# Kernel optimization log

Hardware: AMD Instinct MI355X
Metric: run time of the kernel (lower is better)

The kernel has to match this reference:

```python
import jax, jax.numpy as jnp
import numpy as np
import math

B, S, D, H, F = 2, 2048, 1024, 16, 4096
HD = D // H  # head size 64
EPS = 1e-5


def layernorm(x, g, b):
    mu = jnp.mean(x, axis=-1, keepdims=True)
    var = jnp.mean((x - mu) ** 2, axis=-1, keepdims=True)
    return (x - mu) * jax.lax.rsqrt(var + EPS) * g + b


def new_gelu(x):
    c = math.sqrt(2.0 / math.pi)
    return 0.5 * x * (1.0 + jnp.tanh(c * (x + 0.044715 * x ** 3)))


def setup_inputs() -> dict:
    key = jax.random.key(0)
    ks = jax.random.split(key, 20)
    sc = 0.02
    return {
        "x": jax.random.normal(ks[0], (B, S, D), jnp.float32),
        # per-head q/k/v weights stacked: [H, HD, D] (torch Linear weight layout [out,in])
        "Wq": jax.random.normal(ks[1], (H, HD, D), jnp.float32) * sc,
        "bq": jax.random.normal(ks[2], (H, HD), jnp.float32) * sc,
        "Wk": jax.random.normal(ks[3], (H, HD, D), jnp.float32) * sc,
        "bk": jax.random.normal(ks[4], (H, HD), jnp.float32) * sc,
        "Wv": jax.random.normal(ks[5], (H, HD, D), jnp.float32) * sc,
        "bv": jax.random.normal(ks[6], (H, HD), jnp.float32) * sc,
        "Wo": jax.random.normal(ks[7], (D, D), jnp.float32) * sc,
        "bo": jax.random.normal(ks[8], (D,), jnp.float32) * sc,
        "ln1_g": 1.0 + jax.random.normal(ks[9], (D,), jnp.float32) * sc,
        "ln1_b": jax.random.normal(ks[10], (D,), jnp.float32) * sc,
        "W1": jax.random.normal(ks[11], (F, D), jnp.float32) * sc,
        "b1": jax.random.normal(ks[12], (F,), jnp.float32) * sc,
        "W2": jax.random.normal(ks[13], (D, F), jnp.float32) * sc,
        "b2": jax.random.normal(ks[14], (D,), jnp.float32) * sc,
        "ln2_g": 1.0 + jax.random.normal(ks[15], (D,), jnp.float32) * sc,
        "ln2_b": jax.random.normal(ks[16], (D,), jnp.float32) * sc,
    }


def reference(x, Wq, bq, Wk, bk, Wv, bv, Wo, bo, ln1_g, ln1_b, W1, b1, W2, b2, ln2_g, ln2_b):
    # --- pre-LN multi-head attention (dropout is identity in eval) ---
    h = layernorm(x, ln1_g, ln1_b)
    q = jnp.einsum("bsd,hed->bshe", h, Wq) + bq  # [B,S,H,HD]
    k = jnp.einsum("bsd,hed->bshe", h, Wk) + bk
    v = jnp.einsum("bsd,hed->bshe", h, Wv) + bv
    scores = jnp.einsum("bshe,bthe->bhst", q, k) / math.sqrt(HD)
    probs = jax.nn.softmax(scores, axis=-1)
    attn = jnp.einsum("bhst,bthe->bshe", probs, v).reshape(B, S, D)  # concat heads
    attn = attn @ Wo.T + bo
    x = x + attn
    # --- pre-LN MLP with NewGELU ---
    h2 = layernorm(x, ln2_g, ln2_b)
    mlp = new_gelu(h2 @ W1.T + b1) @ W2.T + b2
    return x + mlp
```

## Files before the change

### kernel.cpp

```cpp
#include <hip/hip_runtime.h>

typedef unsigned short u16;
typedef __attribute__((ext_vector_type(8))) __bf16 bf16x8;
typedef __attribute__((ext_vector_type(4))) __bf16 bf16x4;
typedef __attribute__((ext_vector_type(4))) float f32x4;
typedef __attribute__((ext_vector_type(4))) unsigned short u16x4;

#define AS1 __attribute__((address_space(1)))
#define AS3 __attribute__((address_space(3)))

__device__ __forceinline__ void async_load16(const void* g, void* l) {
  __builtin_amdgcn_global_load_lds((const AS1 void*)g, (AS3 void*)l, 16, 0, 0);
}

__device__ __forceinline__ float exp2_fast(float x) {
#if __has_builtin(__builtin_amdgcn_exp2f)
  return __builtin_amdgcn_exp2f(x);
#else
  return exp2f(x);
#endif
}
__device__ __forceinline__ float rcp_fast(float x) {
#if __has_builtin(__builtin_amdgcn_rcpf)
  return __builtin_amdgcn_rcpf(x);
#else
  return 1.0f / x;
#endif
}

__device__ __forceinline__ u16 f2bf(float f) {
  union { float f; unsigned u; } a; a.f = f;
  unsigned u = a.u;
  u += 0x7fffu + ((u >> 16) & 1u);
  return (u16)(u >> 16);
}
__device__ __forceinline__ u16 bf_bits(float f) {
  union { __bf16 b; u16 u; } c; c.b = (__bf16)f; return c.u;
}
__device__ __forceinline__ float bf2f(u16 h) {
  union { unsigned u; float f; } c; c.u = ((unsigned)h) << 16; return c.f;
}

__global__ __launch_bounds__(256)
void f2b_all(const float* __restrict__ s0, const float* __restrict__ s1,
             const float* __restrict__ s2, const float* __restrict__ s3,
             const float* __restrict__ s4, const float* __restrict__ s5,
             u16* __restrict__ dst) {
  const int i = blockIdx.x * 256 + threadIdx.x;
  const float* s; int off;
  if (i < 1048576) {
    if (i < 262144)      { s = s0; off = i; }
    else if (i < 524288) { s = s1; off = i - 262144; }
    else if (i < 786432) { s = s2; off = i - 524288; }
    else                 { s = s3; off = i - 786432; }
  } else if (i < 2097152) { s = s4; off = i - 1048576; }
  else                    { s = s5; off = i - 2097152; }
  const float4 v = ((const float4*)s)[off];
  u16x4 o; o[0] = f2bf(v.x); o[1] = f2bf(v.y); o[2] = f2bf(v.z); o[3] = f2bf(v.w);
  ((u16x4*)dst)[i] = o;
}

__global__ __launch_bounds__(256)
void ln_kernel(const float* __restrict__ x, const float* __restrict__ g,
               const float* __restrict__ b, u16* __restrict__ out) {
  const int row = blockIdx.x, tid = threadIdx.x;
  const float4 v = ((const float4*)(x + (size_t)row * 1024))[tid];
  float s = v.x + v.y + v.z + v.w;
  float s2 = v.x * v.x + v.y * v.y + v.z * v.z + v.w * v.w;
#pragma unroll
  for (int o = 1; o < 64; o <<= 1) { s += __shfl_xor(s, o); s2 += __shfl_xor(s2, o); }
  __shared__ float red[8];
  const int wave = tid >> 6, lane = tid & 63;
  if (lane == 0) { red[wave] = s; red[wave + 4] = s2; }
  __syncthreads();
  s = red[0] + red[1] + red[2] + red[3];
  s2 = red[4] + red[5] + red[6] + red[7];
  const float mu = s * (1.f / 1024.f);
  const float rstd = rsqrtf(s2 * (1.f / 1024.f) - mu * mu + 1e-5f);
  const float4 gg = ((const float4*)g)[tid];
  const float4 bb = ((const float4*)b)[tid];
  u16x4 o4;
  o4[0] = f2bf((v.x - mu) * rstd * gg.x + bb.x);
  o4[1] = f2bf((v.y - mu) * rstd * gg.y + bb.y);
  o4[2] = f2bf((v.z - mu) * rstd * gg.z + bb.z);
  o4[3] = f2bf((v.w - mu) * rstd * gg.w + bb.w);
  ((u16x4*)(out + (size_t)row * 1024))[tid] = o4;
}

__global__ __launch_bounds__(256)
void ln_fuse(const float* __restrict__ x, const u16* __restrict__ parts,
             const float* __restrict__ bo, const float* __restrict__ g,
             const float* __restrict__ b, float* __restrict__ out,
             u16* __restrict__ hb) {
  const int row = blockIdx.x, tid = threadIdx.x;
  const size_t base = (size_t)row * 1024;
  const int i4 = row * 256 + tid;
  const float4 xv = ((const float4*)(x + base))[tid];
  const u16x4 h0 = ((const u16x4*)parts)[i4];
  const u16x4 h1 = ((const u16x4*)(parts + 4194304))[i4];
  const float4 bv = ((const float4*)bo)[tid];
  float4 t;
  t.x = xv.x + bf2f(h0[0]) + bf2f(h1[0]) + bv.x;
  t.y = xv.y + bf2f(h0[1]) + bf2f(h1[1]) + bv.y;
  t.z = xv.z + bf2f(h0[2]) + bf2f(h1[2]) + bv.z;
  t.w = xv.w + bf2f(h0[3]) + bf2f(h1[3]) + bv.w;
  ((float4*)(out + base))[tid] = t;
  float s = t.x + t.y + t.z + t.w;
  float s2 = t.x * t.x + t.y * t.y + t.z * t.z + t.w * t.w;
#pragma unroll
  for (int o = 1; o < 64; o <<= 1) { s += __shfl_xor(s, o); s2 += __shfl_xor(s2, o); }
  __shared__ float red[8];
  const int wave = tid >> 6, lane = tid & 63;
  if (lane == 0) { red[wave] = s; red[wave + 4] = s2; }
  __syncthreads();
  s = red[0] + red[1] + red[2] + red[3];
  s2 = red[4] + red[5] + red[6] + red[7];
  const float mu = s * (1.f / 1024.f);
  const float rstd = rsqrtf(s2 * (1.f / 1024.f) - mu * mu + 1e-5f);
  const float4 gg = ((const float4*)g)[tid];
  const float4 bb = ((const float4*)b)[tid];
  u16x4 o4;
  o4[0] = f2bf((t.x - mu) * rstd * gg.x + bb.x);
  o4[1] = f2bf((t.y - mu) * rstd * gg.y + bb.y);
  o4[2] = f2bf((t.z - mu) * rstd * gg.z + bb.z);
  o4[3] = f2bf((t.w - mu) * rstd * gg.w + bb.w);
  ((u16x4*)(hb + base))[tid] = o4;
}

__global__ __launch_bounds__(256)
void add4(float* __restrict__ out, const u16* __restrict__ p,
          const float* __restrict__ b2) {
  const int i = blockIdx.x * 256 + threadIdx.x;
  const float4 o = ((const float4*)out)[i];
  const float4 bv = ((const float4*)b2)[i & 255];
  float a0 = o.x + bv.x, a1 = o.y + bv.y, a2 = o.z + bv.z, a3 = o.w + bv.w;
#pragma unroll
  for (int kz = 0; kz < 4; kz++) {
    const u16x4 h = ((const u16x4*)(p + (size_t)kz * 4194304))[i];
    a0 += bf2f(h[0]); a1 += bf2f(h[1]); a2 += bf2f(h[2]); a3 += bf2f(h[3]);
  }
  float4 r; r.x = a0; r.y = a1; r.z = a2; r.w = a3;
  ((float4*)out)[i] = r;
}

template <class Epi>
__global__ __launch_bounds__(256, 2)
void gemm_bt(const u16* __restrict__ A, const u16* __restrict__ Bw,
             int ldk, int K, int NB, Epi epi) {
  __shared__ __align__(16) u16 As[256 * 32];
  __shared__ __align__(16) u16 Bs[128 * 32];
  const int tid = threadIdx.x;
  const int wave = tid >> 6, lane = tid & 63;
  const int quad = lane >> 4, l16 = lane & 15;
  const int id = blockIdx.x;
  const int mb = id & 15;
  const int t = id >> 4;
  const int nb = t % NB;
  const int kz = t / NB;
  const int bm = mb * 256, bn = nb * 128;
  const int wm = wave * 64;

  const int srow = lane >> 2, scol = (lane & 3) * 8;
  const u16* pa[4];
  u16* la[4];
#pragma unroll
  for (int j = 0; j < 4; j++) {
    pa[j] = A + (size_t)(bm + wave * 64 + j * 16 + srow) * ldk + (size_t)kz * K + scol;
    la[j] = &As[wave * 2048 + j * 512];
  }
  const u16* pb[2];
  u16* lb[2];
#pragma unroll
  for (int j = 0; j < 2; j++) {
    pb[j] = Bw + (size_t)(bn + wave * 32 + j * 16 + srow) * ldk + (size_t)kz * K + scol;
    lb[j] = &Bs[wave * 1024 + j * 512];
  }

  const f32x4 fz = {0.f, 0.f, 0.f, 0.f};
  f32x4 acc[4][8];
#pragma unroll
  for (int i = 0; i < 4; i++)
#pragma unroll
    for (int j = 0; j < 8; j++) acc[i][j] = fz;

  for (int k0 = 0; k0 < K; k0 += 32) {
#pragma unroll
    for (int j = 0; j < 4; j++) { async_load16(pa[j], la[j]); pa[j] += 32; }
#pragma unroll
    for (int j = 0; j < 2; j++) { async_load16(pb[j], lb[j]); pb[j] += 32; }
    __syncthreads();
    bf16x8 af[4], bfr[8];
#pragma unroll
    for (int mi = 0; mi < 4; mi++)
      af[mi] = *(const bf16x8*)&As[(wm + mi * 16 + l16) * 32 + quad * 8];
#pragma unroll
    for (int ni = 0; ni < 8; ni++)
      bfr[ni] = *(const bf16x8*)&Bs[(ni * 16 + l16) * 32 + quad * 8];
#pragma unroll
    for (int mi = 0; mi < 4; mi++)
#pragma unroll
      for (int ni = 0; ni < 8; ni++)
        acc[mi][ni] = __builtin_amdgcn_mfma_f32_16x16x32_bf16(af[mi], bfr[ni], acc[mi][ni], 0, 0, 0);
    __syncthreads();
  }
#pragma unroll
  for (int mi = 0; mi < 4; mi++)
#pragma unroll
    for (int ni = 0; ni < 8; ni++)
      epi(bm + wm + mi * 16 + quad * 4, bn + ni * 16 + l16, kz, acc[mi][ni]);
}

struct EpiQKV {
  u16 *q, *k, *vt; const float *bq, *bk, *bv;
  __device__ void operator()(int m0, int n, int, f32x4 v) const {
    const int which = n >> 10, nn = n & 1023;
    const int hh = nn >> 6, e = nn & 63;
    const int bb = m0 >> 11, s0 = m0 & 2047;
    const size_t bh = (size_t)(bb * 16 + hh);
    if (which == 0) {
      const float bias = bq[nn];
      u16* p = &q[(bh * 2048 + s0) * 64 + e];
#pragma unroll
      for (int r = 0; r < 4; r++) p[r * 64] = bf_bits((v[r] + bias) * 0.18033688f);
    } else if (which == 1) {
      const float bias = bk[nn];
      u16* p = &k[(bh * 2048 + s0) * 64 + e];
#pragma unroll
      for (int r = 0; r < 4; r++) p[r * 64] = bf_bits(v[r] + bias);
    } else {
      const float bias = bv[nn];
      bf16x4 pk;
#pragma unroll
      for (int r = 0; r < 4; r++) pk[r] = (__bf16)(v[r] + bias);
      *(bf16x4*)&vt[(bh * 64 + e) * 2048 + s0] = pk;
    }
  }
};
struct EpiPartB {
  u16* p;
  __device__ void operator()(int m0, int n, int kz, f32x4 v) const {
    u16* pp = p + (size_t)kz * 4194304;
#pragma unroll
    for (int r = 0; r < 4; r++) pp[(size_t)(m0 + r) * 1024 + n] = bf_bits(v[r]);
  }
};
struct EpiGelu {
  const float* b1; u16* o;
  __device__ void operator()(int m0, int n, int, f32x4 v) const {
    const float bias = b1[n];
#pragma unroll
    for (int r = 0; r < 4; r++) {
      const float u = v[r] + bias;
      const float z2 = u * (2.3021183f + 0.10294515f * u * u);
      const float d = 1.0f + exp2_fast(-z2);
      o[(size_t)(m0 + r) * 4096 + n] = bf_bits(u * rcp_fast(d));
    }
  }
};

__global__ __launch_bounds__(256)
void attn_kernel(const u16* __restrict__ Q, const u16* __restrict__ K,
                 const u16* __restrict__ Vt, u16* __restrict__ O) {
  __shared__ __align__(16) u16 Ks[64 * 72];
  __shared__ __align__(16) u16 Vs[64 * 72];
  __shared__ __align__(16) u16 Ps[4][32 * 72];
  const int tid = threadIdx.x, wave = tid >> 6, lane = tid & 63;
  const int quad = lane >> 4, l16 = lane & 15;
  const int b = blockIdx.z, h = blockIdx.y, qt = blockIdx.x;
  const size_t bh = (size_t)(b * 16 + h);
  const u16* Qp = Q + bh * (size_t)(2048 * 64);
  const u16* Kp = K + bh * (size_t)(2048 * 64);
  const u16* Vp = Vt + bh * (size_t)(64 * 2048);
  const int q0 = qt * 128 + wave * 32;

  bf16x8 qf[2][2];
#pragma unroll
  for (int rg = 0; rg < 2; rg++) {
    const u16* qrow = &Qp[(size_t)(q0 + rg * 16 + l16) * 64 + quad * 8];
    qf[rg][0] = *(const bf16x8*)qrow;
    qf[rg][1] = *(const bf16x8*)(qrow + 32);
  }

  const int sr = tid >> 2, sc = (tid & 3) * 16;
  const int krow = 4 * (sr & 15) + (sr >> 4);
  const u16* kg = &Kp[(size_t)krow * 64 + sc];
  const u16* vg = &Vp[(size_t)sr * 2048 + sc];
  u16* kl = &Ks[sr * 72 + sc];
  u16* vl = &Vs[sr * 72 + sc];
  u16* Pw = &Ps[wave][0];

  bf16x8 ones;
#pragma unroll
  for (int i = 0; i < 8; i++) ones[i] = (__bf16)1.0f;

  const f32x4 fz = {0.f, 0.f, 0.f, 0.f};
  f32x4 acc[2][4], lsum[2];
#pragma unroll
  for (int rg = 0; rg < 2; rg++) {
    lsum[rg] = fz;
#pragma unroll
    for (int g = 0; g < 4; g++) acc[rg][g] = fz;
  }

  bf16x8 pk0 = *(const bf16x8*)kg, pk1 = *(const bf16x8*)(kg + 8);
  bf16x8 pv0 = *(const bf16x8*)vg, pv1 = *(const bf16x8*)(vg + 8);

  for (int t0 = 0; t0 < 2048; t0 += 64) {
    *(bf16x8*)kl = pk0; *(bf16x8*)(kl + 8) = pk1;
    *(bf16x8*)vl = pv0; *(bf16x8*)(vl + 8) = pv1;
    __syncthreads();
    kg += 64 * 64; vg += 64;
    pk0 = *(const bf16x8*)kg; pk1 = *(const bf16x8*)(kg + 8);
    pv0 = *(const bf16x8*)vg; pv1 = *(const bf16x8*)(vg + 8);

    f32x4 s[2][4];
#pragma unroll
    for (int g = 0; g < 4; g++) {
      const u16* kr = &Ks[(g * 16 + l16) * 72 + quad * 8];
      const bf16x8 kb0 = *(const bf16x8*)kr;
      const bf16x8 kb1 = *(const bf16x8*)(kr + 32);
#pragma unroll
      for (int rg = 0; rg < 2; rg++) {
        f32x4 z = __builtin_amdgcn_mfma_f32_16x16x32_bf16(qf[rg][0], kb0, fz, 0, 0, 0);
        s[rg][g] = __builtin_amdgcn_mfma_f32_16x16x32_bf16(qf[rg][1], kb1, z, 0, 0, 0);
      }
    }
#pragma unroll
    for (int rg = 0; rg < 2; rg++)
#pragma unroll
      for (int r = 0; r < 4; r++) {
        f32x4 pf;
#pragma unroll
        for (int g = 0; g < 4; g++) pf[g] = exp2_fast(s[rg][g][r]);
        const bf16x4 pb = __builtin_convertvector(pf, bf16x4);
        *(bf16x4*)&Pw[(rg * 16 + quad * 4 + r) * 72 + 4 * l16] = pb;
      }
    bf16x8 pa[2][2];
#pragma unroll
    for (int rg = 0; rg < 2; rg++) {
      const u16* pr = &Pw[(rg * 16 + l16) * 72 + quad * 8];
      pa[rg][0] = *(const bf16x8*)pr;
      pa[rg][1] = *(const bf16x8*)(pr + 32);
      lsum[rg] = __builtin_amdgcn_mfma_f32_16x16x32_bf16(pa[rg][0], ones, lsum[rg], 0, 0, 0);
      lsum[rg] = __builtin_amdgcn_mfma_f32_16x16x32_bf16(pa[rg][1], ones, lsum[rg], 0, 0, 0);
    }
#pragma unroll
    for (int g = 0; g < 4; g++) {
      const u16* vr = &Vs[(g * 16 + l16) * 72 + quad * 8];
      const bf16x8 vb0 = *(const bf16x8*)vr;
      const bf16x8 vb1 = *(const bf16x8*)(vr + 32);
#pragma unroll
      for (int rg = 0; rg < 2; rg++) {
        acc[rg][g] = __builtin_amdgcn_mfma_f32_16x16x32_bf16(pa[rg][0], vb0, acc[rg][g], 0, 0, 0);
        acc[rg][g] = __builtin_amdgcn_mfma_f32_16x16x32_bf16(pa[rg][1], vb1, acc[rg][g], 0, 0, 0);
      }
    }
    __syncthreads();
  }
#pragma unroll
  for (int rg = 0; rg < 2; rg++)
#pragma unroll
    for (int r = 0; r < 4; r++) {
      const float inv = rcp_fast(lsum[rg][r]);
      const int s_row = q0 + rg * 16 + quad * 4 + r;
      u16* op = (u16*)&O[((size_t)(b * 2048 + s_row)) * 1024 + h * 64 + l16];
#pragma unroll
      for (int g = 0; g < 4; g++) op[g * 16] = bf_bits(acc[rg][g][r] * inv);
    }
}

extern "C" void kernel_launch(void* const* d_in, const int* in_sizes, int n_in,
                              void* d_out, int out_size, void* d_ws, size_t ws_size,
                              hipStream_t stream) {
  const float* x   = (const float*)d_in[0];
  const float* Wq  = (const float*)d_in[1];
  const float* bq  = (const float*)d_in[2];
  const float* Wk  = (const float*)d_in[3];
  const float* bk  = (const float*)d_in[4];
  const float* Wv  = (const float*)d_in[5];
  const float* bv  = (const float*)d_in[6];
  const float* Wo  = (const float*)d_in[7];
  const float* bo  = (const float*)d_in[8];
  const float* g1  = (const float*)d_in[9];
  const float* be1 = (const float*)d_in[10];
  const float* W1  = (const float*)d_in[11];
  const float* b1  = (const float*)d_in[12];
  const float* W2  = (const float*)d_in[13];
  const float* b2  = (const float*)d_in[14];
  const float* g2  = (const float*)d_in[15];
  const float* be2 = (const float*)d_in[16];
  float* out = (float*)d_out;

  char* w = (char*)d_ws;
  u16* wqkv = (u16*)w; w += (size_t)3072 * 1024 * 2;
  u16* wob  = (u16*)w; w += (size_t)1024 * 1024 * 2;
  u16* w1b  = (u16*)w; w += (size_t)4096 * 1024 * 2;
  u16* w2b  = (u16*)w; w += (size_t)1024 * 4096 * 2;
  u16* hb   = (u16*)w; w += (size_t)4096 * 1024 * 2;
  u16* qb   = (u16*)w; w += (size_t)4096 * 1024 * 2;
  u16* kb   = (u16*)w; w += (size_t)4096 * 1024 * 2;
  u16* vtb  = (u16*)w; w += (size_t)4096 * 1024 * 2;
  u16* atb  = (u16*)w; w += (size_t)4096 * 1024 * 2;
  u16* m1b  = (u16*)w; w += (size_t)4096 * 4096 * 2;

  u16* op_part = m1b;
  u16* ml_part = qb;

  f2b_all<<<12288, 256, 0, stream>>>(Wq, Wk, Wv, Wo, W1, W2, wqkv);

  ln_kernel<<<4096, 256, 0, stream>>>(x, g1, be1, hb);
  gemm_bt<EpiQKV><<<384, 256, 0, stream>>>(hb, wqkv, 1024, 1024, 24,
      EpiQKV{qb, kb, vtb, bq, bk, bv});
  attn_kernel<<<dim3(16, 16, 2), 256, 0, stream>>>(qb, kb, vtb, atb);
  gemm_bt<EpiPartB><<<256, 256, 0, stream>>>(atb, wob, 1024, 512, 8,
      EpiPartB{op_part});
  ln_fuse<<<4096, 256, 0, stream>>>(x, op_part, bo, g2, be2, out, hb);
  gemm_bt<EpiGelu><<<512, 256, 0, stream>>>(hb, w1b, 1024, 1024, 32,
      EpiGelu{b1, m1b});
  gemm_bt<EpiPartB><<<512, 256, 0, stream>>>(m1b, w2b, 4096, 1024, 8,
      EpiPartB{ml_part});
  add4<<<4096, 256, 0, stream>>>(out, ml_part, b2);
}
```

Measured before the change: 360.3 us.

## Halve attention query tile per wave to double grid size

Each wave in the attention kernel now handles 16 query rows instead of 32, so a block covers 64 queries and the grid doubles to 32x16x2 blocks. The goal is more blocks to fill the GPU's compute units, with fewer registers and less shared memory per block so more waves can be resident. In exchange, every K/V tile is loaded from global memory into LDS twice as often overall, and each K/V fragment read from LDS feeds half as many MFMAs.

```diff
diff --git a/kernel.cpp b/kernel.cpp
--- a/kernel.cpp
+++ b/kernel.cpp
@@ -263,7 +263,7 @@
                  const u16* __restrict__ Vt, u16* __restrict__ O) {
   __shared__ __align__(16) u16 Ks[64 * 72];
   __shared__ __align__(16) u16 Vs[64 * 72];
-  __shared__ __align__(16) u16 Ps[4][32 * 72];
+  __shared__ __align__(16) u16 Ps[4][16 * 72];
   const int tid = threadIdx.x, wave = tid >> 6, lane = tid & 63;
   const int quad = lane >> 4, l16 = lane & 15;
   const int b = blockIdx.z, h = blockIdx.y, qt = blockIdx.x;
@@ -271,14 +271,13 @@
   const u16* Qp = Q + bh * (size_t)(2048 * 64);
   const u16* Kp = K + bh * (size_t)(2048 * 64);
   const u16* Vp = Vt + bh * (size_t)(64 * 2048);
-  const int q0 = qt * 128 + wave * 32;
-
-  bf16x8 qf[2][2];
-#pragma unroll
-  for (int rg = 0; rg < 2; rg++) {
-    const u16* qrow = &Qp[(size_t)(q0 + rg * 16 + l16) * 64 + quad * 8];
-    qf[rg][0] = *(const bf16x8*)qrow;
-    qf[rg][1] = *(const bf16x8*)(qrow + 32);
+  const int q0 = qt * 64 + wave * 16;
+
+  bf16x8 qf0, qf1;
+  {
+    const u16* qrow = &Qp[(size_t)(q0 + l16) * 64 + quad * 8];
+    qf0 = *(const bf16x8*)qrow;
+    qf1 = *(const bf16x8*)(qrow + 32);
   }
 
   const int sr = tid >> 2, sc = (tid & 3) * 16;
@@ -294,13 +293,9 @@
   for (int i = 0; i < 8; i++) ones[i] = (__bf16)1.0f;
 
   const f32x4 fz = {0.f, 0.f, 0.f, 0.f};
-  f32x4 acc[2][4], lsum[2];
-#pragma unroll
-  for (int rg = 0; rg < 2; rg++) {
-    lsum[rg] = fz;
-#pragma unroll
-    for (int g = 0; g < 4; g++) acc[rg][g] = fz;
-  }
+  f32x4 acc[4], lsum = fz;
+#pragma unroll
+  for (int g = 0; g < 4; g++) acc[g] = fz;
 
   bf16x8 pk0 = *(const bf16x8*)kg, pk1 = *(const bf16x8*)(kg + 8);
   bf16x8 pv0 = *(const bf16x8*)vg, pv1 = *(const bf16x8*)(vg + 8);
@@ -313,60 +308,49 @@
     pk0 = *(const bf16x8*)kg; pk1 = *(const bf16x8*)(kg + 8);
     pv0 = *(const bf16x8*)vg; pv1 = *(const bf16x8*)(vg + 8);
 
-    f32x4 s[2][4];
+    f32x4 s[4];
 #pragma unroll
     for (int g = 0; g < 4; g++) {
       const u16* kr = &Ks[(g * 16 + l16) * 72 + quad * 8];
       const bf16x8 kb0 = *(const bf16x8*)kr;
       const bf16x8 kb1 = *(const bf16x8*)(kr + 32);
-#pragma unroll
-      for (int rg = 0; rg < 2; rg++) {
-        f32x4 z = __builtin_amdgcn_mfma_f32_16x16x32_bf16(qf[rg][0], kb0, fz, 0, 0, 0);
-        s[rg][g] = __builtin_amdgcn_mfma_f32_16x16x32_bf16(qf[rg][1], kb1, z, 0, 0, 0);
-      }
-    }
-#pragma unroll
-    for (int rg = 0; rg < 2; rg++)
-#pragma unroll
-      for (int r = 0; r < 4; r++) {
-        f32x4 pf;
-#pragma unroll
-        for (int g = 0; g < 4; g++) pf[g] = exp2_fast(s[rg][g][r]);
-        const bf16x4 pb = __builtin_convertvector(pf, bf16x4);
-        *(bf16x4*)&Pw[(rg * 16 + quad * 4 + r) * 72 + 4 * l16] = pb;
-      }
-    bf16x8 pa[2][2];
-#pragma unroll
-    for (int rg = 0; rg < 2; rg++) {
-      const u16* pr = &Pw[(rg * 16 + l16) * 72 + quad * 8];
-      pa[rg][0] = *(const bf16x8*)pr;
-      pa[rg][1] = *(const bf16x8*)(pr + 32);
-      lsum[rg] = __builtin_amdgcn_mfma_f32_16x16x32_bf16(pa[rg][0], ones, lsum[rg], 0, 0, 0);
-      lsum[rg] = __builtin_amdgcn_mfma_f32_16x16x32_bf16(pa[rg][1], ones, lsum[rg], 0, 0, 0);
-    }
+      f32x4 z = __builtin_amdgcn_mfma_f32_16x16x32_bf16(qf0, kb0, fz, 0, 0, 0);
+      s[g] = __builtin_amdgcn_mfma_f32_16x16x32_bf16(qf1, kb1, z, 0, 0, 0);
+    }
+#pragma unroll
+    for (int r = 0; r < 4; r++) {
+      f32x4 pf;
+#pragma unroll
+      for (int g = 0; g < 4; g++) pf[g] = exp2_fast(s[g][r]);
+      const bf16x4 pb = __builtin_convertvector(pf, bf16x4);
+      *(bf16x4*)&Pw[(quad * 4 + r) * 72 + 4 * l16] = pb;
+    }
+    bf16x8 pa0, pa1;
+    {
+      const u16* pr = &Pw[l16 * 72 + quad * 8];
+      pa0 = *(const bf16x8*)pr;
+      pa1 = *(const bf16x8*)(pr + 32);
+    }
+    lsum = __builtin_amdgcn_mfma_f32_16x16x32_bf16(pa0, ones, lsum, 0, 0, 0);
+    lsum = __builtin_amdgcn_mfma_f32_16x16x32_bf16(pa1, ones, lsum, 0, 0, 0);
 #pragma unroll
     for (int g = 0; g < 4; g++) {
       const u16* vr = &Vs[(g * 16 + l16) * 72 + quad * 8];
       const bf16x8 vb0 = *(const bf16x8*)vr;
       const bf16x8 vb1 = *(const bf16x8*)(vr + 32);
-#pragma unroll
-      for (int rg = 0; rg < 2; rg++) {
-        acc[rg][g] = __builtin_amdgcn_mfma_f32_16x16x32_bf16(pa[rg][0], vb0, acc[rg][g], 0, 0, 0);
-        acc[rg][g] = __builtin_amdgcn_mfma_f32_16x16x32_bf16(pa[rg][1], vb1, acc[rg][g], 0, 0, 0);
-      }
+      acc[g] = __builtin_amdgcn_mfma_f32_16x16x32_bf16(pa0, vb0, acc[g], 0, 0, 0);
+      acc[g] = __builtin_amdgcn_mfma_f32_16x16x32_bf16(pa1, vb1, acc[g], 0, 0, 0);
     }
     __syncthreads();
   }
 #pragma unroll
-  for (int rg = 0; rg < 2; rg++)
-#pragma unroll
-    for (int r = 0; r < 4; r++) {
-      const float inv = rcp_fast(lsum[rg][r]);
-      const int s_row = q0 + rg * 16 + quad * 4 + r;
-      u16* op = (u16*)&O[((size_t)(b * 2048 + s_row)) * 1024 + h * 64 + l16];
-#pragma unroll
-      for (int g = 0; g < 4; g++) op[g * 16] = bf_bits(acc[rg][g][r] * inv);
-    }
+  for (int r = 0; r < 4; r++) {
+    const float inv = rcp_fast(lsum[r]);
+    const int s_row = q0 + quad * 4 + r;
+    u16* op = (u16*)&O[((size_t)(b * 2048 + s_row)) * 1024 + h * 64 + l16];
+#pragma unroll
+    for (int g = 0; g < 4; g++) op[g * 16] = bf_bits(acc[g][r] * inv);
+  }
 }
 
 extern "C" void kernel_launch(void* const* d_in, const int* in_sizes, int n_in,
@@ -411,7 +395,7 @@
   ln_kernel<<<4096, 256, 0, stream>>>(x, g1, be1, hb);
   gemm_bt<EpiQKV><<<384, 256, 0, stream>>>(hb, wqkv, 1024, 1024, 24,
       EpiQKV{qb, kb, vtb, bq, bk, bv});
-  attn_kernel<<<dim3(16, 16, 2), 256, 0, stream>>>(qb, kb, vtb, atb);
+  attn_kernel<<<dim3(32, 16, 2), 256, 0, stream>>>(qb, kb, vtb, atb);
   gemm_bt<EpiPartB><<<256, 256, 0, stream>>>(atb, wob, 1024, 512, 8,
       EpiPartB{op_part});
   ln_fuse<<<4096, 256, 0, stream>>>(x, op_part, bo, g2, be2, out, hb);
```

After: 368.2 us. +2.2%, slower.

## Replace GEMM with 8-wave 256x256 double-buffered pipelined kernel and swizzled LDS

Applied to the files above, without the earlier changes.

Replaces the 4-wave 256x128 GEMM, which synchronises on every 32-wide k-step, with an 8-wave 256x256 tile. The new kernel stages 64-wide k tiles through a double-buffered LDS ring with async loads, XOR-swizzles LDS addresses, and uses explicit barriers, waitcnts and setprio to overlap loads with MFMA. The output-projection split-K goes from 2 to 4 parts, and ln_fuse now sums four partials. Attention MFMA sections also gain setprio hints. The larger tiles cut LDS and global traffic per MFMA, at the cost of fewer blocks and more partial-sum traffic for the output projection.

```diff
diff --git a/kernel.cpp b/kernel.cpp
--- a/kernel.cpp
+++ b/kernel.cpp
@@ -96,14 +96,14 @@
   const size_t base = (size_t)row * 1024;
   const int i4 = row * 256 + tid;
   const float4 xv = ((const float4*)(x + base))[tid];
-  const u16x4 h0 = ((const u16x4*)parts)[i4];
-  const u16x4 h1 = ((const u16x4*)(parts + 4194304))[i4];
   const float4 bv = ((const float4*)bo)[tid];
   float4 t;
-  t.x = xv.x + bf2f(h0[0]) + bf2f(h1[0]) + bv.x;
-  t.y = xv.y + bf2f(h0[1]) + bf2f(h1[1]) + bv.y;
-  t.z = xv.z + bf2f(h0[2]) + bf2f(h1[2]) + bv.z;
-  t.w = xv.w + bf2f(h0[3]) + bf2f(h1[3]) + bv.w;
+  t.x = xv.x + bv.x; t.y = xv.y + bv.y; t.z = xv.z + bv.z; t.w = xv.w + bv.w;
+#pragma unroll
+  for (int kz = 0; kz < 4; kz++) {
+    const u16x4 h = ((const u16x4*)(parts + (size_t)kz * 4194304))[i4];
+    t.x += bf2f(h[0]); t.y += bf2f(h[1]); t.z += bf2f(h[2]); t.w += bf2f(h[3]);
+  }
   ((float4*)(out + base))[tid] = t;
   float s = t.x + t.y + t.z + t.w;
   float s2 = t.x * t.x + t.y * t.y + t.z * t.z + t.w * t.w;
@@ -144,70 +144,132 @@
 }
 
 template <class Epi>
-__global__ __launch_bounds__(256, 2)
-void gemm_bt(const u16* __restrict__ A, const u16* __restrict__ Bw,
-             int ldk, int K, int NB, Epi epi) {
-  __shared__ __align__(16) u16 As[256 * 32];
-  __shared__ __align__(16) u16 Bs[128 * 32];
+__global__ __launch_bounds__(512, 2)
+void gemm8(const u16* __restrict__ A, const u16* __restrict__ Bw,
+           int ldk, int K, int NB, Epi epi) {
+  __shared__ __align__(16) u16 lds[65536];
   const int tid = threadIdx.x;
-  const int wave = tid >> 6, lane = tid & 63;
+  const int lane = tid & 63, wave = tid >> 6;
   const int quad = lane >> 4, l16 = lane & 15;
+  const int wmh = wave >> 2, wn = wave & 3;
   const int id = blockIdx.x;
   const int mb = id & 15;
   const int t = id >> 4;
   const int nb = t % NB;
   const int kz = t / NB;
-  const int bm = mb * 256, bn = nb * 128;
-  const int wm = wave * 64;
-
-  const int srow = lane >> 2, scol = (lane & 3) * 8;
-  const u16* pa[4];
-  u16* la[4];
-#pragma unroll
-  for (int j = 0; j < 4; j++) {
-    pa[j] = A + (size_t)(bm + wave * 64 + j * 16 + srow) * ldk + (size_t)kz * K + scol;
-    la[j] = &As[wave * 2048 + j * 512];
-  }
-  const u16* pb[2];
-  u16* lb[2];
-#pragma unroll
-  for (int j = 0; j < 2; j++) {
-    pb[j] = Bw + (size_t)(bn + wave * 32 + j * 16 + srow) * ldk + (size_t)kz * K + scol;
-    lb[j] = &Bs[wave * 1024 + j * 512];
-  }
-
+  const int bm = mb * 256, bn = nb * 256;
+  const int ntile = K >> 6;
+  const int iters = ntile >> 1;
+
+  const int srow = tid >> 3;
+  const int scol = ((tid & 7) * 8) ^ (((tid >> 5) & 1) << 4);
+  const size_t ldkz = (size_t)ldk;
+  const u16* Ag = A + (size_t)(bm + srow) * ldkz + (size_t)kz * K + scol;
+  const u16* Bg = Bw + (size_t)(bn + srow) * ldkz + (size_t)kz * K + scol;
+
+#define STAGE(kt, hf) do { \
+    const u16* gp_ = (((hf) & 2) ? Bg : Ag) + (size_t)(((hf) & 1) * 128) * ldkz + (size_t)(kt) * 64; \
+    u16* lp_ = &lds[(((hf) & 2) ? 32768 : 0) + (((kt) & 1) * 2 + ((hf) & 1)) * 8192 + wave * 512]; \
+    async_load16(gp_, lp_); \
+    async_load16(gp_ + 64 * ldkz, lp_ + 4096); \
+  } while (0)
+#define STG(kt, hf) do { if ((kt) >= 2 && (kt) < ntile) STAGE(kt, hf); } while (0)
+
+  const int qsw = (quad ^ (2 * ((l16 >> 2) & 1))) * 8;
+  const int fro = l16 * 64 + qsw;
+  const u16* aB0 = &lds[(0 * 2 + wmh) * 8192];
+  const u16* aB1 = &lds[(1 * 2 + wmh) * 8192];
+  const u16* bB0 = &lds[32768 + (0 * 2 + (wn >> 1)) * 8192 + (wn & 1) * 4096];
+  const u16* bB1 = &lds[32768 + (1 * 2 + (wn >> 1)) * 8192 + (wn & 1) * 4096];
+
+  bf16x8 aF[4][2], bF[4][2];
   const f32x4 fz = {0.f, 0.f, 0.f, 0.f};
-  f32x4 acc[4][8];
-#pragma unroll
-  for (int i = 0; i < 4; i++)
-#pragma unroll
-    for (int j = 0; j < 8; j++) acc[i][j] = fz;
-
-  for (int k0 = 0; k0 < K; k0 += 32) {
-#pragma unroll
-    for (int j = 0; j < 4; j++) { async_load16(pa[j], la[j]); pa[j] += 32; }
-#pragma unroll
-    for (int j = 0; j < 2; j++) { async_load16(pb[j], lb[j]); pb[j] += 32; }
-    __syncthreads();
-    bf16x8 af[4], bfr[8];
-#pragma unroll
-    for (int mi = 0; mi < 4; mi++)
-      af[mi] = *(const bf16x8*)&As[(wm + mi * 16 + l16) * 32 + quad * 8];
-#pragma unroll
-    for (int ni = 0; ni < 8; ni++)
-      bfr[ni] = *(const bf16x8*)&Bs[(ni * 16 + l16) * 32 + quad * 8];
-#pragma unroll
-    for (int mi = 0; mi < 4; mi++)
-#pragma unroll
-      for (int ni = 0; ni < 8; ni++)
-        acc[mi][ni] = __builtin_amdgcn_mfma_f32_16x16x32_bf16(af[mi], bfr[ni], acc[mi][ni], 0, 0, 0);
-    __syncthreads();
-  }
-#pragma unroll
-  for (int mi = 0; mi < 4; mi++)
-#pragma unroll
-    for (int ni = 0; ni < 8; ni++)
-      epi(bm + wm + mi * 16 + quad * 4, bn + ni * 16 + l16, kz, acc[mi][ni]);
+  f32x4 acc[8][4];
+#pragma unroll
+  for (int m = 0; m < 8; m++)
+#pragma unroll
+    for (int n = 0; n < 4; n++) acc[m][n] = fz;
+
+#define LDAH(ab, mq) do { \
+    aF[0][0] = *(const bf16x8*)&(ab)[fro + ((mq)*4 + 0) * 1024];      \
+    aF[0][1] = *(const bf16x8*)&(ab)[fro + ((mq)*4 + 0) * 1024 + 32]; \
+    aF[1][0] = *(const bf16x8*)&(ab)[fro + ((mq)*4 + 1) * 1024];      \
+    aF[1][1] = *(const bf16x8*)&(ab)[fro + ((mq)*4 + 1) * 1024 + 32]; \
+    aF[2][0] = *(const bf16x8*)&(ab)[fro + ((mq)*4 + 2) * 1024];      \
+    aF[2][1] = *(const bf16x8*)&(ab)[fro + ((mq)*4 + 2) * 1024 + 32]; \
+    aF[3][0] = *(const bf16x8*)&(ab)[fro + ((mq)*4 + 3) * 1024];      \
+    aF[3][1] = *(const bf16x8*)&(ab)[fro + ((mq)*4 + 3) * 1024 + 32]; \
+  } while (0)
+#define LDBH(bb, nq) do { \
+    bF[(nq)*2 + 0][0] = *(const bf16x8*)&(bb)[fro + ((nq)*2 + 0) * 1024];      \
+    bF[(nq)*2 + 0][1] = *(const bf16x8*)&(bb)[fro + ((nq)*2 + 0) * 1024 + 32]; \
+    bF[(nq)*2 + 1][0] = *(const bf16x8*)&(bb)[fro + ((nq)*2 + 1) * 1024];      \
+    bF[(nq)*2 + 1][1] = *(const bf16x8*)&(bb)[fro + ((nq)*2 + 1) * 1024 + 32]; \
+  } while (0)
+#define MFMAQ(mq, nq) \
+  _Pragma("unroll") \
+  for (int mi_ = 0; mi_ < 4; mi_++) \
+    _Pragma("unroll") \
+    for (int ni_ = 0; ni_ < 2; ni_++) \
+      _Pragma("unroll") \
+      for (int kk_ = 0; kk_ < 2; kk_++) \
+        acc[(mq)*4 + mi_][(nq)*2 + ni_] = __builtin_amdgcn_mfma_f32_16x16x32_bf16( \
+            aF[mi_][kk_], bF[(nq)*2 + ni_][kk_], acc[(mq)*4 + mi_][(nq)*2 + ni_], 0, 0, 0);
+#define BODY(mq, nq) do { \
+    __builtin_amdgcn_sched_barrier(0); \
+    __builtin_amdgcn_s_barrier(); \
+    asm volatile("s_waitcnt lgkmcnt(0)" ::: "memory"); \
+    __builtin_amdgcn_sched_barrier(0); \
+    __builtin_amdgcn_s_setprio(1); \
+    MFMAQ(mq, nq); \
+    __builtin_amdgcn_s_setprio(0); \
+    __builtin_amdgcn_sched_barrier(0); \
+    __builtin_amdgcn_s_barrier(); \
+    __builtin_amdgcn_sched_barrier(0); \
+  } while (0)
+
+  STAGE(0, 0); STAGE(0, 1); STAGE(0, 2); STAGE(0, 3);
+  STAGE(1, 0); STAGE(1, 1); STAGE(1, 2); STAGE(1, 3);
+  asm volatile("s_waitcnt vmcnt(8)" ::: "memory");
+  __builtin_amdgcn_s_barrier();
+  __builtin_amdgcn_sched_barrier(0);
+
+  for (int i = 0; i < iters; ++i) {
+    const int k1 = 2 * i + 1, k2 = 2 * i + 2, k3 = 2 * i + 3;
+    const bool last = (i + 1 == iters);
+    LDAH(aB0, 0); LDBH(bB0, 0); STG(k1, 1);
+    BODY(0, 0);
+    LDBH(bB0, 1); STG(k1, 3);
+    BODY(0, 1);
+    LDAH(aB0, 1); STG(k2, 2);
+    BODY(1, 1);
+    STG(k2, 0);
+    if (last) { asm volatile("s_waitcnt vmcnt(0)" ::: "memory"); }
+    else      { asm volatile("s_waitcnt vmcnt(4)" ::: "memory"); }
+    BODY(1, 0);
+    LDAH(aB1, 0); LDBH(bB1, 0); STG(k2, 1);
+    BODY(0, 0);
+    LDBH(bB1, 1); STG(k2, 3);
+    BODY(0, 1);
+    LDAH(aB1, 1); STG(k3, 2);
+    BODY(1, 1);
+    STG(k3, 0);
+    if (last) { asm volatile("s_waitcnt vmcnt(0)" ::: "memory"); }
+    else      { asm volatile("s_waitcnt vmcnt(4)" ::: "memory"); }
+    BODY(1, 0);
+  }
+
+#pragma unroll
+  for (int m = 0; m < 8; m++)
+#pragma unroll
+    for (int n = 0; n < 4; n++)
+      epi(bm + wmh * 128 + m * 16 + quad * 4, bn + wn * 64 + n * 16 + l16, kz, acc[m][n]);
+#undef STAGE
+#undef STG
+#undef LDAH
+#undef LDBH
+#undef MFMAQ
+#undef BODY
 }
 
 struct EpiQKV {
@@ -314,6 +376,7 @@
     pv0 = *(const bf16x8*)vg; pv1 = *(const bf16x8*)(vg + 8);
 
     f32x4 s[2][4];
+    __builtin_amdgcn_s_setprio(1);
 #pragma unroll
     for (int g = 0; g < 4; g++) {
       const u16* kr = &Ks[(g * 16 + l16) * 72 + quad * 8];
@@ -325,6 +388,7 @@
         s[rg][g] = __builtin_amdgcn_mfma_f32_16x16x32_bf16(qf[rg][1], kb1, z, 0, 0, 0);
       }
     }
+    __builtin_amdgcn_s_setprio(0);
 #pragma unroll
     for (int rg = 0; rg < 2; rg++)
 #pragma unroll
@@ -344,6 +408,7 @@
       lsum[rg] = __builtin_amdgcn_mfma_f32_16x16x32_bf16(pa[rg][0], ones, lsum[rg], 0, 0, 0);
       lsum[rg] = __builtin_amdgcn_mfma_f32_16x16x32_bf16(pa[rg][1], ones, lsum[rg], 0, 0, 0);
     }
+    __builtin_amdgcn_s_setprio(1);
 #pragma unroll
     for (int g = 0; g < 4; g++) {
       const u16* vr = &Vs[(g * 16 + l16) * 72 + quad * 8];
@@ -355,6 +420,7 @@
         acc[rg][g] = __builtin_amdgcn_mfma_f32_16x16x32_bf16(pa[rg][1], vb1, acc[rg][g], 0, 0, 0);
       }
     }
+    __builtin_amdgcn_s_setprio(0);
     __syncthreads();
   }
 #pragma unroll
@@ -409,15 +475,15 @@
   f2b_all<<<12288, 256, 0, stream>>>(Wq, Wk, Wv, Wo, W1, W2, wqkv);
 
   ln_kernel<<<4096, 256, 0, stream>>>(x, g1, be1, hb);
-  gemm_bt<EpiQKV><<<384, 256, 0, stream>>>(hb, wqkv, 1024, 1024, 24,
+  gemm8<EpiQKV><<<192, 512, 0, stream>>>(hb, wqkv, 1024, 1024, 12,
       EpiQKV{qb, kb, vtb, bq, bk, bv});
   attn_kernel<<<dim3(16, 16, 2), 256, 0, stream>>>(qb, kb, vtb, atb);
-  gemm_bt<EpiPartB><<<256, 256, 0, stream>>>(atb, wob, 1024, 512, 8,
+  gemm8<EpiPartB><<<256, 512, 0, stream>>>(atb, wob, 1024, 256, 4,
       EpiPartB{op_part});
   ln_fuse<<<4096, 256, 0, stream>>>(x, op_part, bo, g2, be2, out, hb);
-  gemm_bt<EpiGelu><<<512, 256, 0, stream>>>(hb, w1b, 1024, 1024, 32,
+  gemm8<EpiGelu><<<256, 512, 0, stream>>>(hb, w1b, 1024, 1024, 16,
       EpiGelu{b1, m1b});
-  gemm_bt<EpiPartB><<<512, 256, 0, stream>>>(m1b, w2b, 4096, 1024, 8,
+  gemm8<EpiPartB><<<256, 512, 0, stream>>>(m1b, w2b, 4096, 1024, 4,
       EpiPartB{ml_part});
   add4<<<4096, 256, 0, stream>>>(out, ml_part, b2);
 }
```

Result: slower. 446.5 us (+23.9%).
